# Optimization experiments

Measured on AMD Instinct MI355X. Metric: run time of the kernel, lower is better.

Reference implementation:

```python
import jax, jax.numpy as jnp
import numpy as np

B, T = 8, 5
C2, C1, C0 = 128, 256, 512  # in_channels = [C2, C1, C0]


def _ln(x, g, b):
    # LayerNorm over last (channel) axis
    m = jnp.mean(x, axis=-1, keepdims=True)
    v = jnp.var(x, axis=-1, keepdims=True)
    return (x - m) * jax.lax.rsqrt(v + 1e-5) * g + b


def _fuse_branch(x, gc, bc, gr, br, Wcur, Wref, bf, convw, bns, bnb):
    # x: [B, C, T, H, W]
    xt = jnp.transpose(x, (0, 2, 3, 4, 1))            # [B, T, H, W, C] (channel-last, like the permutes)
    cur = xt[:, -1]                                    # [B, H, W, C] last frame
    refs = xt[:, :-1]                                  # [B, T-1, H, W, C]
    # ShiftVSS stand-in: cross-frame fuse with residual (vectorized over T-1 frames)
    cur_proj = jnp.einsum('bhwc,cd->bhwd', _ln(cur, gc, bc), Wcur)        # [B,H,W,C]
    ref_proj = jnp.einsum('bthwc,cd->bthwd', _ln(refs, gr, br), Wref)     # [B,T-1,H,W,C]
    h = cur[:, None] + jax.nn.silu(cur_proj[:, None] + ref_proj + bf)     # [B,T-1,H,W,C]
    # BaseConv 1x1: pointwise conv + folded-BN + SiLU
    y = jax.nn.silu(jnp.einsum('bthwc,cd->bthwd', h, convw) * bns + bnb)  # [B,T-1,H,W,C]
    # fused temporal max + avg pooling (AdaptiveMax/AvgPool3d to T=1)
    pooled = jnp.max(y, axis=1) + jnp.mean(y, axis=1)                     # [B,H,W,C]
    return jnp.transpose(pooled, (0, 3, 1, 2))                            # [B,C,H,W]


def setup_inputs() -> dict:
    key = jax.random.key(0)
    ks = jax.random.split(key, 32)

    def n(k, shape, s=1.0):
        return jax.random.normal(k, shape, dtype=jnp.float32) * s

    d = {}
    d['x2'] = n(ks[0], (B, C2, T, 64, 64))
    d['x1'] = n(ks[1], (B, C1, T, 32, 32))
    d['x0'] = n(ks[2], (B, C0, T, 16, 16))  # unused by forward, kept for signature fidelity
    for i, (p, C) in enumerate([('2', C2), ('1', C1)]):
        o = 3 + i * 4
        d[f'g{p}c'] = jnp.ones((C,), jnp.float32)
        d[f'b{p}c'] = jnp.zeros((C,), jnp.float32)
        d[f'g{p}r'] = jnp.ones((C,), jnp.float32)
        d[f'b{p}r'] = jnp.zeros((C,), jnp.float32)
        d[f'W{p}cur'] = n(ks[o], (C, C), 0.02)
        d[f'W{p}ref'] = n(ks[o + 1], (C, C), 0.02)
        d[f'bias{p}'] = jnp.zeros((C,), jnp.float32)
        d[f'convw{p}'] = n(ks[o + 2], (C, C), 0.02)
        d[f'bns{p}'] = jnp.ones((C,), jnp.float32)
        d[f'bnb{p}'] = jnp.zeros((C,), jnp.float32)
    return d


def reference(x2, x1, x0,
              g2c, b2c, g2r, b2r, W2cur, W2ref, bias2, convw2, bns2, bnb2,
              g1c, b1c, g1r, b1r, W1cur, W1ref, bias1, convw1, bns1, bnb1):
    x2_out = _fuse_branch(x2, g2c, b2c, g2r, b2r, W2cur, W2ref, bias2, convw2, bns2, bnb2)
    x1_out = _fuse_branch(x1, g1c, b1c, g1r, b1r, W1cur, W1ref, bias1, convw1, bns1, bnb1)
    return (x2_out, x1_out)
```

## Files before the change

kernel.cpp:

```cpp
#include <hip/hip_runtime.h>
#include <stdint.h>

#define DI __device__ __forceinline__

typedef __attribute__((ext_vector_type(8))) short short8;
typedef __attribute__((ext_vector_type(4))) float f32x4;

DI float bf2f(unsigned short u){ union{unsigned int i; float f;} v; v.i = ((unsigned int)u)<<16; return v.f; }
DI unsigned short f2bf(float f){ union{float f; unsigned int i;} v; v.f=f; return (unsigned short)((v.i + 0x7fffu + ((v.i>>16)&1u))>>16); }
DI float siluf(float x){ return x/(1.f + __expf(-x)); }
DI f32x4 vzero(){ f32x4 z; z[0]=0.f;z[1]=0.f;z[2]=0.f;z[3]=0.f; return z; }
DI f32x4 vsplat(float x){ f32x4 z; z[0]=x;z[1]=x;z[2]=x;z[3]=x; return z; }

struct PrepArgs {
  const float* W[6];
  const float* g[6];
  unsigned short* Wt[6];
  int C[6];
};

__global__ __launch_bounds__(256) void prep_transpose(PrepArgs a){
  int m = blockIdx.z;
  int C = a.C[m];
  int nt = C >> 5;
  if ((int)blockIdx.x >= nt || (int)blockIdx.y >= nt) return;
  __shared__ float tile[32][33];
  int col = threadIdx.x & 31;
  int rr  = threadIdx.x >> 5;
  const float* W = a.W[m];
  const float* g = a.g[m];
  #pragma unroll
  for (int p=0;p<4;++p){
    int r = rr + p*8;
    int cK = blockIdx.x*32 + r;
    int dN = blockIdx.y*32 + col;
    float v = W[(size_t)cK*C + dN];
    if (g) v *= g[cK];
    tile[r][col] = v;
  }
  __syncthreads();
  unsigned short* Wt = a.Wt[m];
  #pragma unroll
  for (int p=0;p<4;++p){
    int r = rr + p*8;
    int dN = blockIdx.y*32 + r;
    int cK = blockIdx.x*32 + col;
    Wt[(size_t)dN*C + cK] = f2bf(tile[col][r]);
  }
}

struct ColArgs {
  const float* W[4]; const float* g[4]; const float* b[4]; const float* extra[4];
  float* ocs[4]; float* obs[4]; int C[4];
};

__global__ __launch_bounds__(256) void prep_colsum(ColArgs a){
  int j = blockIdx.y;
  int C = a.C[j];
  int d0 = blockIdx.x * 64;
  if (d0 >= C) return;
  int dl = threadIdx.x & 63;
  int g  = threadIdx.x >> 6;
  int d  = d0 + dl;
  const float* W = a.W[j]; const float* gv = a.g[j]; const float* bv = a.b[j];
  float cs = 0.f, bs = 0.f;
  for (int c = g; c < C; c += 4){
    float gc = gv[c], bc = bv[c];
    float w = W[(size_t)c*C + d];
    cs += gc*w;
    bs += bc*w;
  }
  __shared__ float rcs[4][64], rbs[4][64];
  rcs[g][dl] = cs; rbs[g][dl] = bs;
  __syncthreads();
  if (threadIdx.x < 64){
    float c0 = rcs[0][dl]+rcs[1][dl]+rcs[2][dl]+rcs[3][dl];
    float b0 = rbs[0][dl]+rbs[1][dl]+rbs[2][dl]+rbs[3][dl];
    if (a.extra[j]) b0 += a.extra[j][d];
    a.ocs[j][d] = c0;
    a.obs[j][d] = b0;
  }
}


template<int C>
DI short8 readFrag(const short* S, int rowBase, int ks, int lane){
  int row = rowBase + (lane & 15);
  int chunk = (ks*4 + ((lane>>4)&3)) ^ (lane & 7);
  return *(const short8*)((const char*)S + row*(2*C) + chunk*16);
}

template<int C>
DI void stageA_x(const float* __restrict__ xb, int strideC, short* As,
                 float* red, float* smean, float* srstd){
  int tid = threadIdx.x;
  int lane = tid & 63, w = tid >> 6;
  #pragma unroll
  for (int i=0; i<C/16; ++i){
    int ic = i >> 2, ip = i & 3;
    int c  = w*(C/4) + ic*16 + (lane & 15);
    int pq = ip*4 + (lane >> 4);
    f32x4 v = *(const f32x4*)(xb + (size_t)c*strideC + pq*4);
    #pragma unroll
    for (int j=0;j<4;++j){
      int px = pq*4 + j;
      *(unsigned short*)((char*)As + px*(2*C) + (((c>>3) ^ (px&7))*16) + (c&7)*2) = f2bf(v[j]);
    }
  }
  __syncthreads();
  {
    int px = tid & 63, g = tid >> 6;
    constexpr int PER = (C/8)/4;
    float s=0.f, q=0.f;
    #pragma unroll
    for (int k=0;k<PER;++k){
      int ch = g*PER + k;
      short8 v = *(const short8*)((const char*)As + px*(2*C) + ((ch ^ (px&7))*16));
      #pragma unroll
      for (int e=0;e<8;++e){ float f = bf2f((unsigned short)v[e]); s += f; q += f*f; }
    }
    red[g*64+px] = s; red[256+g*64+px] = q;
  }
  __syncthreads();
  if (tid < 64){
    float s=0.f, q=0.f;
    #pragma unroll
    for (int gg=0; gg<4; ++gg){ s += red[gg*64+tid]; q += red[256+gg*64+tid]; }
    float m = s*(1.f/C);
    float var = fmaxf(q*(1.f/C) - m*m, 0.f);
    smean[tid] = m;
    srstd[tid] = rsqrtf(var + 1e-5f);
  }
  __syncthreads();
}

template<int C, int ROWS>
DI void stageCopy(const unsigned short* __restrict__ src, short* dst){
  int tid = threadIdx.x;
  constexpr int CH = C/8;
  constexpr int IT = (ROWS*CH)/256;
  #pragma unroll
  for (int it=0; it<IT; ++it){
    int i = tid + it*256;
    int row = i / CH, ch = i % CH;
    short8 v = *(const short8*)(src + (size_t)row*C + ch*8);
    *(short8*)((char*)dst + row*(2*C) + ((ch ^ (row&7))*16)) = v;
  }
}

template<int C>
DI void mfmaLoop(const short* As, const short* Bs, f32x4 acc[2][4], int lane, int wr, int wc){
  #pragma unroll
  for (int ks=0; ks<C/32; ++ks){
    short8 a0 = readFrag<C>(As, wr*32 +  0, ks, lane);
    short8 a1 = readFrag<C>(As, wr*32 + 16, ks, lane);
    short8 b0 = readFrag<C>(Bs, wc*64 +  0, ks, lane);
    short8 b1 = readFrag<C>(Bs, wc*64 + 16, ks, lane);
    short8 b2 = readFrag<C>(Bs, wc*64 + 32, ks, lane);
    short8 b3 = readFrag<C>(Bs, wc*64 + 48, ks, lane);
    acc[0][0] = __builtin_amdgcn_mfma_f32_16x16x32_bf16(a0,b0,acc[0][0],0,0,0);
    acc[0][1] = __builtin_amdgcn_mfma_f32_16x16x32_bf16(a0,b1,acc[0][1],0,0,0);
    acc[0][2] = __builtin_amdgcn_mfma_f32_16x16x32_bf16(a0,b2,acc[0][2],0,0,0);
    acc[0][3] = __builtin_amdgcn_mfma_f32_16x16x32_bf16(a0,b3,acc[0][3],0,0,0);
    acc[1][0] = __builtin_amdgcn_mfma_f32_16x16x32_bf16(a1,b0,acc[1][0],0,0,0);
    acc[1][1] = __builtin_amdgcn_mfma_f32_16x16x32_bf16(a1,b1,acc[1][1],0,0,0);
    acc[1][2] = __builtin_amdgcn_mfma_f32_16x16x32_bf16(a1,b2,acc[1][2],0,0,0);
    acc[1][3] = __builtin_amdgcn_mfma_f32_16x16x32_bf16(a1,b3,acc[1][3],0,0,0);
  }
}

template<int C>
__global__ __launch_bounds__(256) void k1_curproj(
    const float* __restrict__ x, const unsigned short* __restrict__ Wt,
    const float* __restrict__ colsum, const float* __restrict__ bias,
    unsigned short* __restrict__ Pf, unsigned short* __restrict__ CTf,
    int Npix, int HW){
  constexpr int T = 5;
  constexpr int NY = C/128;
  __shared__ __align__(16) short As[64*C];
  __shared__ __align__(16) short Bs[128*C];
  __shared__ float red[512];
  __shared__ float smean[64], srstd[64];

  int ny = blockIdx.y;
  int n0 = ny*128;
  int px0 = blockIdx.x*64;
  int b = px0 / HW, hw0 = px0 % HW;
  const float* xb = x + ((size_t)b*C*T + (T-1))*HW + hw0;

  stageCopy<C,128>(Wt + (size_t)n0*C, Bs);
  stageA_x<C>(xb, T*HW, As, red, smean, srstd);

  int tid = threadIdx.x, lane = tid&63, wid = tid>>6, wr = wid>>1, wc = wid&1, hi = lane>>4;

  float csv[4], biv[4];
  #pragma unroll
  for (int nf=0;nf<4;++nf){ int d = n0 + wc*64 + nf*16 + (lane&15); csv[nf]=colsum[d]; biv[nf]=bias[d]; }

  f32x4 acc[2][4];
  #pragma unroll
  for (int i=0;i<2;++i)
    #pragma unroll
    for (int j=0;j<4;++j) acc[i][j] = vzero();
  mfmaLoop<C>(As, Bs, acc, lane, wr, wc);

  size_t fb = ((size_t)(px0>>6)*NY + ny)*4;
  #pragma unroll
  for (int k=0;k<4;++k){
    short8 pv, cv;
    int dg = n0 + wc*64 + k*16 + (lane&15);
    #pragma unroll
    for (int mf=0;mf<2;++mf)
      #pragma unroll
      for (int r=0;r<4;++r){
        int pl = wr*32+mf*16+hi*4+r;
        float P = srstd[pl]*(acc[mf][k][r] - smean[pl]*csv[k]) + biv[k];
        pv[mf*4+r] = (short)f2bf(P);
        cv[mf*4+r] = (short)*(const unsigned short*)((const char*)As + pl*(2*C) + (((dg>>3)^(pl&7))*16) + (dg&7)*2);
      }
    *(short8*)(Pf  + ((fb+k)*256 + tid)*8) = pv;
    *(short8*)(CTf + ((fb+k)*256 + tid)*8) = cv;
  }
}

template<int C>
__global__ __launch_bounds__(256) void k2_refproj(
    const float* __restrict__ x, const unsigned short* __restrict__ Wt,
    const float* __restrict__ colsum, const float* __restrict__ biasRf,
    const unsigned short* __restrict__ Pf, const unsigned short* __restrict__ CTf,
    unsigned short* __restrict__ hout, int Npix, int HW){
  constexpr int T = 5;
  constexpr int NY = C/128;
  __shared__ __align__(16) short As[64*C];
  __shared__ __align__(16) short Bs[128*C];
  __shared__ float red[512];
  __shared__ float smean[64], srstd[64];

  int ny = blockIdx.y;
  int n0 = ny*128;
  int px0 = blockIdx.x*64;
  int t = blockIdx.z;
  int b = px0 / HW, hw0 = px0 % HW;
  const float* xb = x + ((size_t)b*C*T + t)*HW + hw0;

  stageCopy<C,128>(Wt + (size_t)n0*C, Bs);
  stageA_x<C>(xb, T*HW, As, red, smean, srstd);

  int tid = threadIdx.x, lane = tid&63, wid = tid>>6, wr = wid>>1, wc = wid&1, hi = lane>>4;

  float csv[4], biv[4];
  #pragma unroll
  for (int nf=0;nf<4;++nf){ int d = n0 + wc*64 + nf*16 + (lane&15); csv[nf]=colsum[d]; biv[nf]=biasRf[d]; }

  f32x4 acc[2][4];
  #pragma unroll
  for (int i=0;i<2;++i)
    #pragma unroll
    for (int j=0;j<4;++j) acc[i][j] = vzero();
  mfmaLoop<C>(As, Bs, acc, lane, wr, wc);

  size_t fb = ((size_t)(px0>>6)*NY + ny)*4;
  short8 pv[4], cv[4];
  #pragma unroll
  for (int k=0;k<4;++k){
    pv[k] = *(const short8*)(Pf  + ((fb+k)*256 + tid)*8);
    cv[k] = *(const short8*)(CTf + ((fb+k)*256 + tid)*8);
  }
  __syncthreads();
  short* h_lds = As;
  #pragma unroll
  for (int nf=0;nf<4;++nf){
    int dl = wc*64 + nf*16 + (lane&15);
    #pragma unroll
    for (int mf=0;mf<2;++mf)
      #pragma unroll
      for (int r=0;r<4;++r){
        int pl = wr*32+mf*16+hi*4+r;
        float pre = srstd[pl]*(acc[mf][nf][r]-smean[pl]*csv[nf]) + biv[nf] + bf2f((unsigned short)pv[nf][mf*4+r]);
        float h = bf2f((unsigned short)cv[nf][mf*4+r]) + siluf(pre);
        *(unsigned short*)((char*)h_lds + pl*256 + (((dl>>3)^(pl&7))*16) + (dl&7)*2) = f2bf(h);
      }
  }
  __syncthreads();
  #pragma unroll
  for (int it=0; it<4; ++it){
    int i = tid + it*256;
    int row = i >> 4, ch = i & 15;
    short8 v = *(const short8*)((const char*)h_lds + row*256 + ((ch ^ (row&7))*16));
    *(short8*)(hout + ((size_t)t*Npix + px0 + row)*C + n0 + ch*8) = v;
  }
}

template<int C>
__global__ __launch_bounds__(256) void k3_conv(
    const unsigned short* __restrict__ h, const unsigned short* __restrict__ WtV,
    const float* __restrict__ bns, const float* __restrict__ bnb,
    float* __restrict__ out, int Npix, int HW){
  constexpr int PB = 133;
  constexpr int AsBytes = 64*C*2;
  constexpr int PoolBytes = 64*PB*4;
  constexpr int U = (AsBytes > PoolBytes) ? AsBytes : PoolBytes;
  __shared__ __align__(16) char uni[U];
  __shared__ __align__(16) short Bs[128*C];
  short* As = (short*)uni;
  float* pool = (float*)uni;

  int n0 = blockIdx.y*128;
  int px0 = blockIdx.x*64;
  int b = px0 / HW, hw0 = px0 % HW;
  int tid = threadIdx.x, lane = tid&63, wid = tid>>6, wr = wid>>1, wc = wid&1, hi = lane>>4;

  stageCopy<C,128>(WtV + (size_t)n0*C, Bs);

  f32x4 mx[2][4], sm[2][4];
  #pragma unroll
  for (int i=0;i<2;++i)
    #pragma unroll
    for (int j=0;j<4;++j){ mx[i][j] = vsplat(-3.0e38f); sm[i][j] = vzero(); }

  for (int t=0; t<4; ++t){
    __syncthreads();
    stageCopy<C,64>(h + ((size_t)t*Npix + px0)*C, As);
    __syncthreads();
    f32x4 acc[2][4];
    #pragma unroll
    for (int i=0;i<2;++i)
      #pragma unroll
      for (int j=0;j<4;++j) acc[i][j] = vzero();
    mfmaLoop<C>(As, Bs, acc, lane, wr, wc);
    #pragma unroll
    for (int nf=0; nf<4; ++nf){
      int d = n0 + wc*64 + nf*16 + (lane&15);
      float s_ = bns[d], b_ = bnb[d];
      #pragma unroll
      for (int mf=0; mf<2; ++mf){
        #pragma unroll
        for (int r=0; r<4; ++r){
          float y = siluf(acc[mf][nf][r]*s_ + b_);
          mx[mf][nf][r] = fmaxf(mx[mf][nf][r], y);
          sm[mf][nf][r] += y;
        }
      }
    }
  }

  __syncthreads();
  #pragma unroll
  for (int nf=0; nf<4; ++nf){
    int dl = wc*64 + nf*16 + (lane&15);
    #pragma unroll
    for (int mf=0; mf<2; ++mf){
      #pragma unroll
      for (int r=0; r<4; ++r){
        int pl = wr*32 + mf*16 + hi*4 + r;
        pool[pl*PB + dl] = mx[mf][nf][r] + 0.25f*sm[mf][nf][r];
      }
    }
  }
  __syncthreads();

  #pragma unroll
  for (int it=0; it<8; ++it){
    int i = tid + it*256;
    int dl = i >> 4;
    int pq = (i & 15) * 4;
    f32x4 vv;
    #pragma unroll
    for (int k=0;k<4;++k) vv[k] = pool[(pq+k)*PB + dl];
    *(f32x4*)(out + (size_t)(b*C + n0 + dl)*HW + hw0 + pq) = vv;
  }
}

extern "C" void kernel_launch(void* const* d_in, const int* in_sizes, int n_in,
                              void* d_out, int out_size, void* d_ws, size_t ws_size,
                              hipStream_t stream) {
  (void)in_sizes; (void)n_in; (void)out_size; (void)ws_size;
  const float* x2    = (const float*)d_in[0];
  const float* x1    = (const float*)d_in[1];
  const float* g2c   = (const float*)d_in[3];
  const float* b2c   = (const float*)d_in[4];
  const float* g2r   = (const float*)d_in[5];
  const float* b2r   = (const float*)d_in[6];
  const float* W2cur = (const float*)d_in[7];
  const float* W2ref = (const float*)d_in[8];
  const float* bias2 = (const float*)d_in[9];
  const float* convw2= (const float*)d_in[10];
  const float* bns2  = (const float*)d_in[11];
  const float* bnb2  = (const float*)d_in[12];
  const float* g1c   = (const float*)d_in[13];
  const float* b1c   = (const float*)d_in[14];
  const float* g1r   = (const float*)d_in[15];
  const float* b1r   = (const float*)d_in[16];
  const float* W1cur = (const float*)d_in[17];
  const float* W1ref = (const float*)d_in[18];
  const float* bias1 = (const float*)d_in[19];
  const float* convw1= (const float*)d_in[20];
  const float* bns1  = (const float*)d_in[21];
  const float* bnb1  = (const float*)d_in[22];

  const int C2 = 128, C1 = 256;
  const int NP2 = 8*64*64, NP1 = 8*32*32;
  const int HW2 = 4096, HW1 = 1024;

  char* ws = (char*)d_ws;
  size_t off = 0;
  auto alloc = [&](size_t bytes){ size_t o = off; off = (off + bytes + 255) & ~(size_t)255; return o; };
  size_t oWtC2 = alloc((size_t)C2*C2*2), oWtR2 = alloc((size_t)C2*C2*2), oWtV2 = alloc((size_t)C2*C2*2);
  size_t oWtC1 = alloc((size_t)C1*C1*2), oWtR1 = alloc((size_t)C1*C1*2), oWtV1 = alloc((size_t)C1*C1*2);
  size_t oColC2 = alloc(C2*4), oBiasC2 = alloc(C2*4), oColR2 = alloc(C2*4), oBiasR2 = alloc(C2*4);
  size_t oColC1 = alloc(C1*4), oBiasC1 = alloc(C1*4), oColR1 = alloc(C1*4), oBiasR1 = alloc(C1*4);
  size_t oP2  = alloc((size_t)NP2*C2*2);
  size_t oCT2 = alloc((size_t)NP2*C2*2);
  size_t oH2  = alloc((size_t)4*NP2*C2*2);
  size_t oP1  = alloc((size_t)NP1*C1*2);
  size_t oCT1 = alloc((size_t)NP1*C1*2);
  size_t oH1  = alloc((size_t)4*NP1*C1*2);

  unsigned short* WtC2 = (unsigned short*)(ws + oWtC2);
  unsigned short* WtR2 = (unsigned short*)(ws + oWtR2);
  unsigned short* WtV2 = (unsigned short*)(ws + oWtV2);
  unsigned short* WtC1 = (unsigned short*)(ws + oWtC1);
  unsigned short* WtR1 = (unsigned short*)(ws + oWtR1);
  unsigned short* WtV1 = (unsigned short*)(ws + oWtV1);
  float* ColC2 = (float*)(ws + oColC2); float* BiasC2 = (float*)(ws + oBiasC2);
  float* ColR2 = (float*)(ws + oColR2); float* BiasR2 = (float*)(ws + oBiasR2);
  float* ColC1 = (float*)(ws + oColC1); float* BiasC1 = (float*)(ws + oBiasC1);
  float* ColR1 = (float*)(ws + oColR1); float* BiasR1 = (float*)(ws + oBiasR1);
  unsigned short* P2  = (unsigned short*)(ws + oP2);
  unsigned short* CT2 = (unsigned short*)(ws + oCT2);
  unsigned short* H2  = (unsigned short*)(ws + oH2);
  unsigned short* P1  = (unsigned short*)(ws + oP1);
  unsigned short* CT1 = (unsigned short*)(ws + oCT1);
  unsigned short* H1  = (unsigned short*)(ws + oH1);

  PrepArgs pa;
  pa.W[0]=W2cur;  pa.g[0]=g2c;     pa.Wt[0]=WtC2; pa.C[0]=C2;
  pa.W[1]=W2ref;  pa.g[1]=g2r;     pa.Wt[1]=WtR2; pa.C[1]=C2;
  pa.W[2]=convw2; pa.g[2]=nullptr; pa.Wt[2]=WtV2; pa.C[2]=C2;
  pa.W[3]=W1cur;  pa.g[3]=g1c;     pa.Wt[3]=WtC1; pa.C[3]=C1;
  pa.W[4]=W1ref;  pa.g[4]=g1r;     pa.Wt[4]=WtR1; pa.C[4]=C1;
  pa.W[5]=convw1; pa.g[5]=nullptr; pa.Wt[5]=WtV1; pa.C[5]=C1;
  prep_transpose<<<dim3(8,8,6), 256, 0, stream>>>(pa);

  ColArgs ca;
  ca.W[0]=W2cur; ca.g[0]=g2c; ca.b[0]=b2c; ca.extra[0]=nullptr; ca.ocs[0]=ColC2; ca.obs[0]=BiasC2; ca.C[0]=C2;
  ca.W[1]=W2ref; ca.g[1]=g2r; ca.b[1]=b2r; ca.extra[1]=bias2;   ca.ocs[1]=ColR2; ca.obs[1]=BiasR2; ca.C[1]=C2;
  ca.W[2]=W1cur; ca.g[2]=g1c; ca.b[2]=b1c; ca.extra[2]=nullptr; ca.ocs[2]=ColC1; ca.obs[2]=BiasC1; ca.C[2]=C1;
  ca.W[3]=W1ref; ca.g[3]=g1r; ca.b[3]=b1r; ca.extra[3]=bias1;   ca.ocs[3]=ColR1; ca.obs[3]=BiasR1; ca.C[3]=C1;
  prep_colsum<<<dim3(4, 4), 256, 0, stream>>>(ca);

  float* out2 = (float*)d_out;
  float* out1 = out2 + (size_t)8*C2*HW2;

  k1_curproj<128><<<dim3(NP2/64, 1),    256, 0, stream>>>(x2, WtC2, ColC2, BiasC2, P2, CT2, NP2, HW2);
  k1_curproj<256><<<dim3(NP1/64, 2),    256, 0, stream>>>(x1, WtC1, ColC1, BiasC1, P1, CT1, NP1, HW1);
  k2_refproj<128><<<dim3(NP2/64, 1, 4), 256, 0, stream>>>(x2, WtR2, ColR2, BiasR2, P2, CT2, H2, NP2, HW2);
  k2_refproj<256><<<dim3(NP1/64, 2, 4), 256, 0, stream>>>(x1, WtR1, ColR1, BiasR1, P1, CT1, H1, NP1, HW1);
  k3_conv<128><<<dim3(NP2/64, 1),       256, 0, stream>>>(H2, WtV2, bns2, bnb2, out2, NP2, HW2);
  k3_conv<256><<<dim3(NP1/64, 2),       256, 0, stream>>>(H1, WtV1, bns1, bnb1, out1, NP1, HW1);
}
```

Measured before the change: 142.4 us.

## Fuse cur-proj, ref-proj, conv and pooling into one per-tile kernel

Replaces the three per-branch kernels (current-frame projection, reference projection, pointwise conv with pooling) with a single kernel per branch. Each block keeps its 64-pixel tile's current-frame projection and residual in registers and the h activations in LDS. It runs all four reference frames and the conv in-block, which removes the global round trips for P, CT and H. In exchange each block restages every weight matrix from global on every frame and needs a large LDS footprint (up to 128KB for C=256). It also launches fewer blocks, which lowers occupancy and parallelism.

```diff
diff --git a/kernel.cpp b/kernel.cpp
--- a/kernel.cpp
+++ b/kernel.cpp
@@ -169,158 +169,51 @@
   }
 }
 
-template<int C>
-__global__ __launch_bounds__(256) void k1_curproj(
-    const float* __restrict__ x, const unsigned short* __restrict__ Wt,
-    const float* __restrict__ colsum, const float* __restrict__ bias,
-    unsigned short* __restrict__ Pf, unsigned short* __restrict__ CTf,
-    int Npix, int HW){
+template<int C, int MINW>
+__global__ __launch_bounds__(256, MINW) void fused_branch(
+    const float* __restrict__ x,
+    const unsigned short* __restrict__ WtCur,
+    const unsigned short* __restrict__ WtRef,
+    const unsigned short* __restrict__ WtConv,
+    const float* __restrict__ colC, const float* __restrict__ biasC,
+    const float* __restrict__ colR, const float* __restrict__ biasR,
+    const float* __restrict__ bns, const float* __restrict__ bnb,
+    float* __restrict__ out, int HW){
   constexpr int T = 5;
-  constexpr int NY = C/128;
-  __shared__ __align__(16) short As[64*C];
-  __shared__ __align__(16) short Bs[128*C];
+  constexpr int NH = C/128;
+  __shared__ __align__(16) char Lraw[512*C];
+  short* As = (short*)Lraw;
+  short* Hs = (short*)(Lraw + 128*C);
+  short* Bs = (short*)(Lraw + 256*C);
+  float* pool = (float*)Lraw;
   __shared__ float red[512];
   __shared__ float smean[64], srstd[64];
 
-  int ny = blockIdx.y;
-  int n0 = ny*128;
-  int px0 = blockIdx.x*64;
-  int b = px0 / HW, hw0 = px0 % HW;
-  const float* xb = x + ((size_t)b*C*T + (T-1))*HW + hw0;
-
-  stageCopy<C,128>(Wt + (size_t)n0*C, Bs);
-  stageA_x<C>(xb, T*HW, As, red, smean, srstd);
-
-  int tid = threadIdx.x, lane = tid&63, wid = tid>>6, wr = wid>>1, wc = wid&1, hi = lane>>4;
-
-  float csv[4], biv[4];
-  #pragma unroll
-  for (int nf=0;nf<4;++nf){ int d = n0 + wc*64 + nf*16 + (lane&15); csv[nf]=colsum[d]; biv[nf]=bias[d]; }
-
-  f32x4 acc[2][4];
-  #pragma unroll
-  for (int i=0;i<2;++i)
-    #pragma unroll
-    for (int j=0;j<4;++j) acc[i][j] = vzero();
-  mfmaLoop<C>(As, Bs, acc, lane, wr, wc);
-
-  size_t fb = ((size_t)(px0>>6)*NY + ny)*4;
-  #pragma unroll
-  for (int k=0;k<4;++k){
-    short8 pv, cv;
-    int dg = n0 + wc*64 + k*16 + (lane&15);
-    #pragma unroll
-    for (int mf=0;mf<2;++mf)
-      #pragma unroll
-      for (int r=0;r<4;++r){
-        int pl = wr*32+mf*16+hi*4+r;
-        float P = srstd[pl]*(acc[mf][k][r] - smean[pl]*csv[k]) + biv[k];
-        pv[mf*4+r] = (short)f2bf(P);
-        cv[mf*4+r] = (short)*(const unsigned short*)((const char*)As + pl*(2*C) + (((dg>>3)^(pl&7))*16) + (dg&7)*2);
-      }
-    *(short8*)(Pf  + ((fb+k)*256 + tid)*8) = pv;
-    *(short8*)(CTf + ((fb+k)*256 + tid)*8) = cv;
-  }
-}
-
-template<int C>
-__global__ __launch_bounds__(256) void k2_refproj(
-    const float* __restrict__ x, const unsigned short* __restrict__ Wt,
-    const float* __restrict__ colsum, const float* __restrict__ biasRf,
-    const unsigned short* __restrict__ Pf, const unsigned short* __restrict__ CTf,
-    unsigned short* __restrict__ hout, int Npix, int HW){
-  constexpr int T = 5;
-  constexpr int NY = C/128;
-  __shared__ __align__(16) short As[64*C];
-  __shared__ __align__(16) short Bs[128*C];
-  __shared__ float red[512];
-  __shared__ float smean[64], srstd[64];
-
-  int ny = blockIdx.y;
-  int n0 = ny*128;
-  int px0 = blockIdx.x*64;
-  int t = blockIdx.z;
-  int b = px0 / HW, hw0 = px0 % HW;
-  const float* xb = x + ((size_t)b*C*T + t)*HW + hw0;
-
-  stageCopy<C,128>(Wt + (size_t)n0*C, Bs);
-  stageA_x<C>(xb, T*HW, As, red, smean, srstd);
-
-  int tid = threadIdx.x, lane = tid&63, wid = tid>>6, wr = wid>>1, wc = wid&1, hi = lane>>4;
-
-  float csv[4], biv[4];
-  #pragma unroll
-  for (int nf=0;nf<4;++nf){ int d = n0 + wc*64 + nf*16 + (lane&15); csv[nf]=colsum[d]; biv[nf]=biasRf[d]; }
-
-  f32x4 acc[2][4];
-  #pragma unroll
-  for (int i=0;i<2;++i)
-    #pragma unroll
-    for (int j=0;j<4;++j) acc[i][j] = vzero();
-  mfmaLoop<C>(As, Bs, acc, lane, wr, wc);
-
-  size_t fb = ((size_t)(px0>>6)*NY + ny)*4;
-  short8 pv[4], cv[4];
-  #pragma unroll
-  for (int k=0;k<4;++k){
-    pv[k] = *(const short8*)(Pf  + ((fb+k)*256 + tid)*8);
-    cv[k] = *(const short8*)(CTf + ((fb+k)*256 + tid)*8);
-  }
-  __syncthreads();
-  short* h_lds = As;
-  #pragma unroll
-  for (int nf=0;nf<4;++nf){
-    int dl = wc*64 + nf*16 + (lane&15);
-    #pragma unroll
-    for (int mf=0;mf<2;++mf)
-      #pragma unroll
-      for (int r=0;r<4;++r){
-        int pl = wr*32+mf*16+hi*4+r;
-        float pre = srstd[pl]*(acc[mf][nf][r]-smean[pl]*csv[nf]) + biv[nf] + bf2f((unsigned short)pv[nf][mf*4+r]);
-        float h = bf2f((unsigned short)cv[nf][mf*4+r]) + siluf(pre);
-        *(unsigned short*)((char*)h_lds + pl*256 + (((dl>>3)^(pl&7))*16) + (dl&7)*2) = f2bf(h);
-      }
-  }
-  __syncthreads();
-  #pragma unroll
-  for (int it=0; it<4; ++it){
-    int i = tid + it*256;
-    int row = i >> 4, ch = i & 15;
-    short8 v = *(const short8*)((const char*)h_lds + row*256 + ((ch ^ (row&7))*16));
-    *(short8*)(hout + ((size_t)t*Npix + px0 + row)*C + n0 + ch*8) = v;
-  }
-}
-
-template<int C>
-__global__ __launch_bounds__(256) void k3_conv(
-    const unsigned short* __restrict__ h, const unsigned short* __restrict__ WtV,
-    const float* __restrict__ bns, const float* __restrict__ bnb,
-    float* __restrict__ out, int Npix, int HW){
-  constexpr int PB = 133;
-  constexpr int AsBytes = 64*C*2;
-  constexpr int PoolBytes = 64*PB*4;
-  constexpr int U = (AsBytes > PoolBytes) ? AsBytes : PoolBytes;
-  __shared__ __align__(16) char uni[U];
-  __shared__ __align__(16) short Bs[128*C];
-  short* As = (short*)uni;
-  float* pool = (float*)uni;
-
-  int n0 = blockIdx.y*128;
   int px0 = blockIdx.x*64;
   int b = px0 / HW, hw0 = px0 % HW;
   int tid = threadIdx.x, lane = tid&63, wid = tid>>6, wr = wid>>1, wc = wid&1, hi = lane>>4;
 
-  stageCopy<C,128>(WtV + (size_t)n0*C, Bs);
-
-  f32x4 mx[2][4], sm[2][4];
+  float csR[NH*4], biR[NH*4], scv[NH*4], sbv[NH*4];
+  #pragma unroll
+  for (int h=0;h<NH;++h)
+    #pragma unroll
+    for (int k=0;k<4;++k){
+      int d = h*128 + wc*64 + k*16 + (lane&15);
+      csR[h*4+k] = colR[d]; biR[h*4+k] = biasR[d];
+      scv[h*4+k] = bns[d];  sbv[h*4+k] = bnb[d];
+    }
+
+  short8 pv[NH*4], cv[NH*4];
+  f32x4 mx[2][NH*4], sm[2][NH*4];
   #pragma unroll
   for (int i=0;i<2;++i)
     #pragma unroll
-    for (int j=0;j<4;++j){ mx[i][j] = vsplat(-3.0e38f); sm[i][j] = vzero(); }
-
-  for (int t=0; t<4; ++t){
-    __syncthreads();
-    stageCopy<C,64>(h + ((size_t)t*Npix + px0)*C, As);
+    for (int j=0;j<NH*4;++j){ mx[i][j] = vsplat(-3.0e38f); sm[i][j] = vzero(); }
+
+  stageA_x<C>(x + ((size_t)b*C*T + (T-1))*HW + hw0, T*HW, As, red, smean, srstd);
+  #pragma unroll
+  for (int h=0;h<NH;++h){
+    stageCopy<C,128>(WtCur + (size_t)h*128*C, Bs);
     __syncthreads();
     f32x4 acc[2][4];
     #pragma unroll
@@ -329,45 +222,100 @@
       for (int j=0;j<4;++j) acc[i][j] = vzero();
     mfmaLoop<C>(As, Bs, acc, lane, wr, wc);
     #pragma unroll
-    for (int nf=0; nf<4; ++nf){
-      int d = n0 + wc*64 + nf*16 + (lane&15);
-      float s_ = bns[d], b_ = bnb[d];
-      #pragma unroll
-      for (int mf=0; mf<2; ++mf){
-        #pragma unroll
-        for (int r=0; r<4; ++r){
-          float y = siluf(acc[mf][nf][r]*s_ + b_);
-          mx[mf][nf][r] = fmaxf(mx[mf][nf][r], y);
-          sm[mf][nf][r] += y;
+    for (int k=0;k<4;++k){
+      int dg = h*128 + wc*64 + k*16 + (lane&15);
+      float cs = colC[dg], bi = biasC[dg];
+      short8 p8, c8;
+      #pragma unroll
+      for (int mf=0;mf<2;++mf)
+        #pragma unroll
+        for (int r=0;r<4;++r){
+          int pl = wr*32 + mf*16 + hi*4 + r;
+          float P = srstd[pl]*(acc[mf][k][r] - smean[pl]*cs) + bi;
+          p8[mf*4+r] = (short)f2bf(P);
+          c8[mf*4+r] = (short)*(const unsigned short*)((const char*)As + pl*(2*C) + (((dg>>3)^(pl&7))*16) + (dg&7)*2);
         }
+      pv[h*4+k] = p8; cv[h*4+k] = c8;
+    }
+    __syncthreads();
+  }
+
+  for (int t=0;t<4;++t){
+    stageA_x<C>(x + ((size_t)b*C*T + t)*HW + hw0, T*HW, As, red, smean, srstd);
+    #pragma unroll
+    for (int h=0;h<NH;++h){
+      stageCopy<C,128>(WtRef + (size_t)h*128*C, Bs);
+      __syncthreads();
+      f32x4 acc[2][4];
+      #pragma unroll
+      for (int i=0;i<2;++i)
+        #pragma unroll
+        for (int j=0;j<4;++j) acc[i][j] = vzero();
+      mfmaLoop<C>(As, Bs, acc, lane, wr, wc);
+      #pragma unroll
+      for (int k=0;k<4;++k){
+        int dg = h*128 + wc*64 + k*16 + (lane&15);
+        #pragma unroll
+        for (int mf=0;mf<2;++mf)
+          #pragma unroll
+          for (int r=0;r<4;++r){
+            int pl = wr*32 + mf*16 + hi*4 + r;
+            float pre = srstd[pl]*(acc[mf][k][r] - smean[pl]*csR[h*4+k]) + biR[h*4+k] + bf2f((unsigned short)pv[h*4+k][mf*4+r]);
+            float hv = bf2f((unsigned short)cv[h*4+k][mf*4+r]) + siluf(pre);
+            *(unsigned short*)((char*)Hs + pl*(2*C) + (((dg>>3)^(pl&7))*16) + (dg&7)*2) = f2bf(hv);
+          }
       }
-    }
-  }
-
-  __syncthreads();
-  #pragma unroll
-  for (int nf=0; nf<4; ++nf){
-    int dl = wc*64 + nf*16 + (lane&15);
-    #pragma unroll
-    for (int mf=0; mf<2; ++mf){
-      #pragma unroll
-      for (int r=0; r<4; ++r){
-        int pl = wr*32 + mf*16 + hi*4 + r;
-        pool[pl*PB + dl] = mx[mf][nf][r] + 0.25f*sm[mf][nf][r];
+      __syncthreads();
+    }
+    #pragma unroll
+    for (int h=0;h<NH;++h){
+      stageCopy<C,128>(WtConv + (size_t)h*128*C, Bs);
+      __syncthreads();
+      f32x4 acc[2][4];
+      #pragma unroll
+      for (int i=0;i<2;++i)
+        #pragma unroll
+        for (int j=0;j<4;++j) acc[i][j] = vzero();
+      mfmaLoop<C>(Hs, Bs, acc, lane, wr, wc);
+      #pragma unroll
+      for (int k=0;k<4;++k){
+        float s_ = scv[h*4+k], b_ = sbv[h*4+k];
+        #pragma unroll
+        for (int mf=0;mf<2;++mf)
+          #pragma unroll
+          for (int r=0;r<4;++r){
+            float y = siluf(acc[mf][k][r]*s_ + b_);
+            mx[mf][h*4+k][r] = fmaxf(mx[mf][h*4+k][r], y);
+            sm[mf][h*4+k][r] += y;
+          }
       }
-    }
-  }
-  __syncthreads();
-
-  #pragma unroll
-  for (int it=0; it<8; ++it){
+      __syncthreads();
+    }
+  }
+
+  #pragma unroll
+  for (int h=0;h<NH;++h)
+    #pragma unroll
+    for (int k=0;k<4;++k){
+      int dl = h*128 + wc*64 + k*16 + (lane&15);
+      #pragma unroll
+      for (int mf=0;mf<2;++mf)
+        #pragma unroll
+        for (int r=0;r<4;++r){
+          int pl = wr*32 + mf*16 + hi*4 + r;
+          pool[pl*(C+1) + dl] = mx[mf][h*4+k][r] + 0.25f*sm[mf][h*4+k][r];
+        }
+    }
+  __syncthreads();
+  #pragma unroll
+  for (int it=0; it<C/16; ++it){
     int i = tid + it*256;
     int dl = i >> 4;
     int pq = (i & 15) * 4;
     f32x4 vv;
     #pragma unroll
-    for (int k=0;k<4;++k) vv[k] = pool[(pq+k)*PB + dl];
-    *(f32x4*)(out + (size_t)(b*C + n0 + dl)*HW + hw0 + pq) = vv;
+    for (int k=0;k<4;++k) vv[k] = pool[(pq+k)*(C+1) + dl];
+    *(f32x4*)(out + (size_t)(b*C + dl)*HW + hw0 + pq) = vv;
   }
 }
 
@@ -409,12 +357,6 @@
   size_t oWtC1 = alloc((size_t)C1*C1*2), oWtR1 = alloc((size_t)C1*C1*2), oWtV1 = alloc((size_t)C1*C1*2);
   size_t oColC2 = alloc(C2*4), oBiasC2 = alloc(C2*4), oColR2 = alloc(C2*4), oBiasR2 = alloc(C2*4);
   size_t oColC1 = alloc(C1*4), oBiasC1 = alloc(C1*4), oColR1 = alloc(C1*4), oBiasR1 = alloc(C1*4);
-  size_t oP2  = alloc((size_t)NP2*C2*2);
-  size_t oCT2 = alloc((size_t)NP2*C2*2);
-  size_t oH2  = alloc((size_t)4*NP2*C2*2);
-  size_t oP1  = alloc((size_t)NP1*C1*2);
-  size_t oCT1 = alloc((size_t)NP1*C1*2);
-  size_t oH1  = alloc((size_t)4*NP1*C1*2);
 
   unsigned short* WtC2 = (unsigned short*)(ws + oWtC2);
   unsigned short* WtR2 = (unsigned short*)(ws + oWtR2);
@@ -426,12 +368,6 @@
   float* ColR2 = (float*)(ws + oColR2); float* BiasR2 = (float*)(ws + oBiasR2);
   float* ColC1 = (float*)(ws + oColC1); float* BiasC1 = (float*)(ws + oBiasC1);
   float* ColR1 = (float*)(ws + oColR1); float* BiasR1 = (float*)(ws + oBiasR1);
-  unsigned short* P2  = (unsigned short*)(ws + oP2);
-  unsigned short* CT2 = (unsigned short*)(ws + oCT2);
-  unsigned short* H2  = (unsigned short*)(ws + oH2);
-  unsigned short* P1  = (unsigned short*)(ws + oP1);
-  unsigned short* CT1 = (unsigned short*)(ws + oCT1);
-  unsigned short* H1  = (unsigned short*)(ws + oH1);
 
   PrepArgs pa;
   pa.W[0]=W2cur;  pa.g[0]=g2c;     pa.Wt[0]=WtC2; pa.C[0]=C2;
@@ -452,10 +388,8 @@
   float* out2 = (float*)d_out;
   float* out1 = out2 + (size_t)8*C2*HW2;
 
-  k1_curproj<128><<<dim3(NP2/64, 1),    256, 0, stream>>>(x2, WtC2, ColC2, BiasC2, P2, CT2, NP2, HW2);
-  k1_curproj<256><<<dim3(NP1/64, 2),    256, 0, stream>>>(x1, WtC1, ColC1, BiasC1, P1, CT1, NP1, HW1);
-  k2_refproj<128><<<dim3(NP2/64, 1, 4), 256, 0, stream>>>(x2, WtR2, ColR2, BiasR2, P2, CT2, H2, NP2, HW2);
-  k2_refproj<256><<<dim3(NP1/64, 2, 4), 256, 0, stream>>>(x1, WtR1, ColR1, BiasR1, P1, CT1, H1, NP1, HW1);
-  k3_conv<128><<<dim3(NP2/64, 1),       256, 0, stream>>>(H2, WtV2, bns2, bnb2, out2, NP2, HW2);
-  k3_conv<256><<<dim3(NP1/64, 2),       256, 0, stream>>>(H1, WtV1, bns1, bnb1, out1, NP1, HW1);
-}
+  fused_branch<128,2><<<NP2/64, 256, 0, stream>>>(
+      x2, WtC2, WtR2, WtV2, ColC2, BiasC2, ColR2, BiasR2, bns2, bnb2, out2, HW2);
+  fused_branch<256,1><<<NP1/64, 256, 0, stream>>>(
+      x1, WtC1, WtR1, WtV1, ColC1, BiasC1, ColR1, BiasR1, bns1, bnb1, out1, HW1);
+}
```

After: 544.8 us. +282.6%, slower.
